# Kernel tuning notes

Hardware: AMD Instinct MI355X
Metric: run time of the kernel (lower is better)

The kernel has to match this reference:

```python
import jax, jax.numpy as jnp
import numpy as np

INPUT_DIM, DIM_K, DIM_V = 1024, 512, 512

def setup_inputs() -> dict:
    key = jax.random.key(0)
    kx, kq, kk, kv = jax.random.split(key, 4)
    x = jax.random.normal(kx, (4, 4096, INPUT_DIM), dtype=jnp.float32)
    s = 1.0 / np.sqrt(INPUT_DIM)
    Wq = jax.random.normal(kq, (INPUT_DIM, DIM_K), dtype=jnp.float32) * s
    Wk = jax.random.normal(kk, (INPUT_DIM, DIM_K), dtype=jnp.float32) * s
    Wv = jax.random.normal(kv, (INPUT_DIM, DIM_V), dtype=jnp.float32) * s
    return {"x": x, "Wq": Wq, "Wk": Wk, "Wv": Wv}

def reference(x, Wq, Wk, Wv):
    # x: [b, n, d_in]; bias-free projections
    Q = jnp.einsum('bnd,dk->bnk', x, Wq)
    K = jnp.einsum('bnd,dk->bnk', x, Wk)
    V = jnp.einsum('bnd,dv->bnv', x, Wv)
    scale = 1.0 / np.sqrt(Wq.shape[1])
    scores = jnp.einsum('bqk,bnk->bqn', Q, K) * scale  # [b, n, n]
    atten = jax.nn.softmax(scores, axis=-1)
    return jnp.einsum('bqn,bnv->bqv', atten, V)
```

## Files before the change

### kernel.cpp

```cpp
#include <hip/hip_runtime.h>
#include <hip/hip_bf16.h>


typedef __attribute__((ext_vector_type(8))) short bf16x8;
typedef __attribute__((ext_vector_type(4))) float floatx4;

static __device__ __forceinline__ unsigned short f2bf(float f) {
    unsigned int u = __builtin_bit_cast(unsigned int, f);
    return (unsigned short)((u + 0x7fffu + ((u >> 16) & 1u)) >> 16);
}

static __device__ __forceinline__ void gl2lds16(const unsigned short* g, unsigned short* l) {
    __builtin_amdgcn_global_load_lds(
        (const __attribute__((address_space(1))) unsigned int*)g,
        (__attribute__((address_space(3))) unsigned int*)l, 16, 0, 0);
}

#define BAR() __asm__ volatile("s_barrier" ::: "memory")
#define WVMC4() __asm__ volatile("s_waitcnt vmcnt(4)" ::: "memory")
#define WVMC0() __asm__ volatile("s_waitcnt vmcnt(0)" ::: "memory")
#define WLGKM0() __asm__ volatile("s_waitcnt lgkmcnt(0)" ::: "memory")
#define WALL() __asm__ volatile("s_waitcnt vmcnt(0) lgkmcnt(0)" ::: "memory")

__global__ __launch_bounds__(256) void cvt_bf16(const float* __restrict__ X,
                                                unsigned short* __restrict__ Y, int n4) {
    int i = blockIdx.x * 256 + threadIdx.x;
    if (i < n4) {
        float4 v = reinterpret_cast<const float4*>(X)[i];
        ushort4 o;
        o.x = f2bf(v.x); o.y = f2bf(v.y); o.z = f2bf(v.z); o.w = f2bf(v.w);
        reinterpret_cast<ushort4*>(Y)[i] = o;
    }
}

__global__ __launch_bounds__(256) void transpose_w(const float* __restrict__ W,
                                                   unsigned short* __restrict__ Wt, int off) {
    __shared__ float tile[32][33];
    int n0 = blockIdx.x * 32;
    int k0 = blockIdx.y * 32;
    int tx = threadIdx.x & 31, ty = threadIdx.x >> 5;
    for (int i = 0; i < 32; i += 8)
        tile[ty + i][tx] = W[(size_t)(k0 + ty + i) * 512 + n0 + tx];
    __syncthreads();
    for (int i = 0; i < 32; i += 8)
        Wt[(size_t)(off + n0 + ty + i) * 1024 + k0 + tx] = f2bf(tile[tx][ty + i]);
}

__global__ __launch_bounds__(256) void gemm_qkv(const unsigned short* __restrict__ A,
                                                const unsigned short* __restrict__ Bt,
                                                unsigned short* __restrict__ Qb,
                                                unsigned short* __restrict__ Kfr,
                                                unsigned short* __restrict__ Vfr) {
    __shared__ unsigned short As[128 * 32];
    __shared__ unsigned short Bs[128 * 32];
    const int K = 1024;
    const int L = blockIdx.x;
    const int mt = ((L & 7) << 4) | ((L >> 3) & 15);
    const int nt = L >> 7;
    const int m0 = mt * 128, n0 = nt * 128;
    const int tid = threadIdx.x;
    const int lane = tid & 63, wave = tid >> 6;
    const int wm = (wave >> 1) * 64, wn = (wave & 1) * 64;
    const int quad = lane >> 4, l15 = lane & 15;

    floatx4 acc[4][4] = {};
    const int srow = tid >> 2, scol = (tid & 3) * 8;

    for (int kt = 0; kt < K; kt += 32) {
        const unsigned short* ga = A + (size_t)(m0 + srow) * K + kt + scol;
        const unsigned short* gb = Bt + (size_t)(n0 + srow) * K + kt + scol;
        gl2lds16(ga, As + tid * 8);
        gl2lds16(ga + (size_t)64 * K, As + 2048 + tid * 8);
        gl2lds16(gb, Bs + tid * 8);
        gl2lds16(gb + (size_t)64 * K, Bs + 2048 + tid * 8);
        __syncthreads();
        bf16x8 af[4], bfr[4];
#pragma unroll
        for (int i = 0; i < 4; i++)
            af[i] = *reinterpret_cast<const bf16x8*>(As + (wm + i * 16 + l15) * 32 + quad * 8);
#pragma unroll
        for (int j = 0; j < 4; j++)
            bfr[j] = *reinterpret_cast<const bf16x8*>(Bs + (wn + j * 16 + l15) * 32 + quad * 8);
#pragma unroll
        for (int i = 0; i < 4; i++)
#pragma unroll
            for (int j = 0; j < 4; j++)
                acc[i][j] = __builtin_amdgcn_mfma_f32_16x16x32_bf16(af[i], bfr[j], acc[i][j], 0, 0, 0);
        __syncthreads();
    }

    const float qscale = 0.044194173824159216f;
#pragma unroll
    for (int i = 0; i < 4; i++)
#pragma unroll
        for (int j = 0; j < 4; j++)
#pragma unroll
            for (int r = 0; r < 4; r++) {
                int row = m0 + wm + i * 16 + quad * 4 + r;
                int col = n0 + wn + j * 16 + l15;
                if (n0 < 512) {
                    Qb[(size_t)row * 512 + col] = f2bf(acc[i][j][r] * qscale);
                } else if (n0 < 1024) {
                    int d = col - 512;
                    size_t base = ((size_t)((row >> 12) * 128 + ((row & 4095) >> 5))) << 14;
                    int off = ((d >> 5) * 2 + ((row >> 4) & 1)) * 512 +
                              (((d >> 3) & 3) * 16 + (row & 15)) * 8 + (d & 7);
                    Kfr[base + off] = f2bf(acc[i][j][r]);
                } else {
                    int d = col - 1024;
                    size_t base = ((size_t)((row >> 12) * 128 + ((row & 4095) >> 5))) << 14;
                    int off = (d >> 4) * 512 +
                              (((row & 31) >> 3) * 16 + (d & 15)) * 8 + (row & 7);
                    Vfr[base + off] = f2bf(acc[i][j][r]);
                }
            }
}

__global__ __launch_bounds__(512, 2) void attn(const unsigned short* __restrict__ Qg,
                                               const unsigned short* __restrict__ Kf,
                                               const unsigned short* __restrict__ Vf,
                                               float* __restrict__ O0,
                                               float* __restrict__ O1,
                                               float* __restrict__ lpart) {
    __shared__ unsigned short Kb[16384];
    __shared__ unsigned short Vb[3][16384];
    __shared__ unsigned short Ps[2][8][512];

    const int L = blockIdx.x;
    const int b = L & 3;
    const int h = (L >> 2) & 1;
    const int q0 = (L >> 3) * 128;
    const int tid = threadIdx.x;
    const int lane = tid & 63, wave = tid >> 6;
    const int quad = lane >> 4, l15 = lane & 15;
    const int qh = wave >> 2, dq = wave & 3;

    const unsigned short* KfB = Kf + ((size_t)b << 21);
    const unsigned short* VfB = Vf + ((size_t)b << 21);
    float* Od = (h == 0) ? O0 : O1;

    bf16x8 qf[16];
    {
        const unsigned short* qrow =
            Qg + (size_t)(b * 4096 + q0 + wave * 16 + l15) * 512 + quad * 8;
#pragma unroll
        for (int ks = 0; ks < 16; ks++)
            qf[ks] = *reinterpret_cast<const bf16x8*>(qrow + ks * 32);
    }
    WALL();

    floatx4 o[4][8];
#pragma unroll
    for (int g = 0; g < 4; g++)
#pragma unroll
        for (int n2 = 0; n2 < 8; n2++) o[g][n2] = floatx4{0.f, 0.f, 0.f, 0.f};
    float lp = 0.f;

    const int kt0 = h * 64;
    {
        const unsigned short* gK = KfB + ((size_t)kt0 << 14);
#pragma unroll
        for (int i = 0; i < 4; i++)
            gl2lds16(gK + (i * 512 + tid) * 8, &Kb[(i * 512 + tid) * 8]);
    }

    int vs = 0;
    for (int it = 0; it < 64; it++) {
        {
            const unsigned short* gV = VfB + ((size_t)(kt0 + it) << 14);
#pragma unroll
            for (int i = 0; i < 4; i++)
                gl2lds16(gV + (i * 512 + tid) * 8, &Vb[vs][(i * 512 + tid) * 8]);
        }
        WVMC4();
        BAR();

        const unsigned short* Kc = &Kb[0];
        floatx4 s00 = {0.f,0.f,0.f,0.f}, s01 = {0.f,0.f,0.f,0.f};
        floatx4 s10 = {0.f,0.f,0.f,0.f}, s11 = {0.f,0.f,0.f,0.f};
        __builtin_amdgcn_s_setprio(1);
#pragma unroll
        for (int ks = 0; ks < 16; ks += 2) {
            bf16x8 k0a = *reinterpret_cast<const bf16x8*>(Kc + (2 * ks + 0) * 512 + lane * 8);
            bf16x8 k1a = *reinterpret_cast<const bf16x8*>(Kc + (2 * ks + 1) * 512 + lane * 8);
            bf16x8 k0b = *reinterpret_cast<const bf16x8*>(Kc + (2 * ks + 2) * 512 + lane * 8);
            bf16x8 k1b = *reinterpret_cast<const bf16x8*>(Kc + (2 * ks + 3) * 512 + lane * 8);
            s00 = __builtin_amdgcn_mfma_f32_16x16x32_bf16(k0a, qf[ks], s00, 0, 0, 0);
            s10 = __builtin_amdgcn_mfma_f32_16x16x32_bf16(k1a, qf[ks], s10, 0, 0, 0);
            s01 = __builtin_amdgcn_mfma_f32_16x16x32_bf16(k0b, qf[ks + 1], s01, 0, 0, 0);
            s11 = __builtin_amdgcn_mfma_f32_16x16x32_bf16(k1b, qf[ks + 1], s11, 0, 0, 0);
        }
        __builtin_amdgcn_s_setprio(0);
        floatx4 s0v = s00 + s01, s1v = s10 + s11;

        {
            float p0[4], p1[4];
#pragma unroll
            for (int r = 0; r < 4; r++) {
                p0[r] = __expf(s0v[r] - 16.0f);
                p1[r] = __expf(s1v[r] - 16.0f);
                lp += p0[r] + p1[r];
            }
            unsigned int a0, a1, b0, b1;
            asm("v_cvt_pk_bf16_f32 %0, %1, %2" : "=v"(a0) : "v"(p0[0]), "v"(p0[1]));
            asm("v_cvt_pk_bf16_f32 %0, %1, %2" : "=v"(a1) : "v"(p0[2]), "v"(p0[3]));
            asm("v_cvt_pk_bf16_f32 %0, %1, %2" : "=v"(b0) : "v"(p1[0]), "v"(p1[1]));
            asm("v_cvt_pk_bf16_f32 %0, %1, %2" : "=v"(b1) : "v"(p1[2]), "v"(p1[3]));
            unsigned short* Pw = &Ps[it & 1][wave][0];
            const int wo = (quad >> 1) * 128 + l15 * 8 + (quad & 1) * 4;
            *reinterpret_cast<uint2*>(Pw + wo)       = uint2{a0, a1};
            *reinterpret_cast<uint2*>(Pw + wo + 256) = uint2{b0, b1};
        }
        WLGKM0();
        WVMC0();
        BAR();

        {
            const unsigned short* gK = KfB + ((size_t)(kt0 + ((it + 1) & 63)) << 14);
#pragma unroll
            for (int i = 0; i < 4; i++)
                gl2lds16(gK + (i * 512 + tid) * 8, &Kb[(i * 512 + tid) * 8]);
        }

        const unsigned short* Vc = &Vb[vs][0];
        bf16x8 vfr[8];
#pragma unroll
        for (int n2 = 0; n2 < 8; n2++)
            vfr[n2] = *reinterpret_cast<const bf16x8*>(Vc + (dq * 8 + n2) * 512 + lane * 8);
        __builtin_amdgcn_s_setprio(1);
#pragma unroll
        for (int g = 0; g < 4; g++) {
            bf16x8 pf = *reinterpret_cast<const bf16x8*>(&Ps[it & 1][qh * 4 + g][0] + lane * 8);
#pragma unroll
            for (int n2 = 0; n2 < 8; n2++)
                o[g][n2] = __builtin_amdgcn_mfma_f32_16x16x32_bf16(pf, vfr[n2], o[g][n2], 0, 0, 0);
        }
        __builtin_amdgcn_s_setprio(0);

        vs = (vs == 2) ? 0 : vs + 1;
    }
    WALL();

    lp += __shfl_xor(lp, 16);
    lp += __shfl_xor(lp, 32);
    if (quad == 0)
        lpart[h * 16384 + b * 4096 + q0 + wave * 16 + l15] = lp;

#pragma unroll
    for (int g = 0; g < 4; g++)
#pragma unroll
        for (int r = 0; r < 4; r++) {
            size_t rowoff = (size_t)(b * 4096 + q0 + qh * 64 + g * 16 + quad * 4 + r) * 512
                            + dq * 128 + l15;
#pragma unroll
            for (int n2 = 0; n2 < 8; n2++)
                Od[rowoff + n2 * 16] = o[g][n2][r];
        }
}

__global__ __launch_bounds__(256) void combine(float* __restrict__ Out,
                                               const float* __restrict__ O1,
                                               const float* __restrict__ lpart) {
    int i = blockIdx.x * 256 + threadIdx.x;
    int row = i >> 7;
    float inv = 1.0f / (lpart[row] + lpart[16384 + row]);
    float4 a = reinterpret_cast<const float4*>(Out)[i];
    float4 c = reinterpret_cast<const float4*>(O1)[i];
    float4 r;
    r.x = (a.x + c.x) * inv;
    r.y = (a.y + c.y) * inv;
    r.z = (a.z + c.z) * inv;
    r.w = (a.w + c.w) * inv;
    reinterpret_cast<float4*>(Out)[i] = r;
}

extern "C" void kernel_launch(void* const* d_in, const int* in_sizes, int n_in,
                              void* d_out, int out_size, void* d_ws, size_t ws_size,
                              hipStream_t stream) {
    const float* x  = (const float*)d_in[0];
    const float* Wq = (const float*)d_in[1];
    const float* Wk = (const float*)d_in[2];
    const float* Wv = (const float*)d_in[3];

    char* ws = (char*)d_ws;
    unsigned short* Wtall = (unsigned short*)(ws);
    unsigned short* Qb  = (unsigned short*)(ws + (3u << 20));
    unsigned short* Kfr = (unsigned short*)(ws + (19u << 20));
    unsigned short* Vfr = (unsigned short*)(ws + (35u << 20));
    unsigned short* xb  = (unsigned short*)(ws + (51u << 20));
    float* O1    = (float*)(ws + (51u << 20));
    float* lpart = (float*)(ws + (83u << 20));

    dim3 tb(256);
    cvt_bf16<<<dim3(16384), tb, 0, stream>>>(x, xb, 16384 * 1024 / 4);
    transpose_w<<<dim3(16, 32), tb, 0, stream>>>(Wq, Wtall, 0);
    transpose_w<<<dim3(16, 32), tb, 0, stream>>>(Wk, Wtall, 512);
    transpose_w<<<dim3(16, 32), tb, 0, stream>>>(Wv, Wtall, 1024);
    gemm_qkv<<<dim3(1536), tb, 0, stream>>>(xb, Wtall, Qb, Kfr, Vfr);
    attn<<<dim3(256), dim3(512), 0, stream>>>(Qb, Kfr, Vfr, (float*)d_out, O1, lpart);
    combine<<<dim3(8192), tb, 0, stream>>>((float*)d_out, O1, lpart);
}
```

Baseline: 341.3 us.

## Rewrite QKV GEMM with 256x192 tiles, swizzled LDS and multi-stage prefetch

The QKV projection GEMM moves from 128x128 tiles with a single-buffered K loop of 32 to 256x192 tiles with 512 threads and a K step of 64. A operands are triple-buffered and B operands double-buffered in an XOR-swizzled LDS layout, with staged global-to-LDS loads interleaved between MFMA phases and wave priority raised around the MFMA blocks. The three weight-transpose launches are merged into one 3D-grid launch. The aim is to hide global load latency, cut LDS bank conflicts and raise arithmetic intensity, at the cost of more LDS, more registers and more complex barrier sequencing.

```diff
diff --git a/kernel.cpp b/kernel.cpp
--- a/kernel.cpp
+++ b/kernel.cpp
@@ -33,9 +33,13 @@
     }
 }
 
-__global__ __launch_bounds__(256) void transpose_w(const float* __restrict__ W,
-                                                   unsigned short* __restrict__ Wt, int off) {
+__global__ __launch_bounds__(256) void transpose_w3(const float* __restrict__ Wq,
+                                                    const float* __restrict__ Wk,
+                                                    const float* __restrict__ Wv,
+                                                    unsigned short* __restrict__ Wt) {
     __shared__ float tile[32][33];
+    const float* W = (blockIdx.z == 0) ? Wq : (blockIdx.z == 1) ? Wk : Wv;
+    const int off = blockIdx.z << 9;
     int n0 = blockIdx.x * 32;
     int k0 = blockIdx.y * 32;
     int tx = threadIdx.x & 31, ty = threadIdx.x >> 5;
@@ -46,72 +50,153 @@
         Wt[(size_t)(off + n0 + ty + i) * 1024 + k0 + tx] = f2bf(tile[tx][ty + i]);
 }
 
-__global__ __launch_bounds__(256) void gemm_qkv(const unsigned short* __restrict__ A,
-                                                const unsigned short* __restrict__ Bt,
-                                                unsigned short* __restrict__ Qb,
-                                                unsigned short* __restrict__ Kfr,
-                                                unsigned short* __restrict__ Vfr) {
-    __shared__ unsigned short As[128 * 32];
-    __shared__ unsigned short Bs[128 * 32];
-    const int K = 1024;
+__global__ __launch_bounds__(512, 2) void gemm_qkv(const unsigned short* __restrict__ A,
+                                                   const unsigned short* __restrict__ Bt,
+                                                   unsigned short* __restrict__ Qb,
+                                                   unsigned short* __restrict__ Kfr,
+                                                   unsigned short* __restrict__ Vfr) {
+    __shared__ unsigned short AsU[3 * 16384];
+    __shared__ unsigned short BsU[2 * 12288];
+
     const int L = blockIdx.x;
-    const int mt = ((L & 7) << 4) | ((L >> 3) & 15);
-    const int nt = L >> 7;
-    const int m0 = mt * 128, n0 = nt * 128;
+    const int i6 = L >> 3;
+    const int mt = ((L & 7) << 3) | (i6 >> 3);
+    const int nt = i6 & 7;
+    const int m0 = mt << 8, n0 = nt * 192;
     const int tid = threadIdx.x;
     const int lane = tid & 63, wave = tid >> 6;
-    const int wm = (wave >> 1) * 64, wn = (wave & 1) * 64;
+    const int wmi = wave >> 2, wni = wave & 3;
     const int quad = lane >> 4, l15 = lane & 15;
 
-    floatx4 acc[4][4] = {};
-    const int srow = tid >> 2, scol = (tid & 3) * 8;
-
-    for (int kt = 0; kt < K; kt += 32) {
-        const unsigned short* ga = A + (size_t)(m0 + srow) * K + kt + scol;
-        const unsigned short* gb = Bt + (size_t)(n0 + srow) * K + kt + scol;
-        gl2lds16(ga, As + tid * 8);
-        gl2lds16(ga + (size_t)64 * K, As + 2048 + tid * 8);
-        gl2lds16(gb, Bs + tid * 8);
-        gl2lds16(gb + (size_t)64 * K, Bs + 2048 + tid * 8);
-        __syncthreads();
-        bf16x8 af[4], bfr[4];
-#pragma unroll
-        for (int i = 0; i < 4; i++)
-            af[i] = *reinterpret_cast<const bf16x8*>(As + (wm + i * 16 + l15) * 32 + quad * 8);
-#pragma unroll
-        for (int j = 0; j < 4; j++)
-            bfr[j] = *reinterpret_cast<const bf16x8*>(Bs + (wn + j * 16 + l15) * 32 + quad * 8);
-#pragma unroll
-        for (int i = 0; i < 4; i++)
-#pragma unroll
-            for (int j = 0; j < 4; j++)
-                acc[i][j] = __builtin_amdgcn_mfma_f32_16x16x32_bf16(af[i], bfr[j], acc[i][j], 0, 0, 0);
-        __syncthreads();
-    }
+    const int srow = tid >> 3;
+    const int sslot = (tid & 7) ^ ((tid >> 3) & 7);
+
+    auto stageA = [&](int slot, int ktile, int c) {
+        const unsigned short* src =
+            A + (size_t)(m0 + c * 64 + srow) * 1024 + (ktile << 6) + sslot * 8;
+        gl2lds16(src, AsU + slot * 16384 + c * 4096 + tid * 8);
+    };
+    auto stageB = [&](int slot, int ktile, int c) {
+        const unsigned short* src =
+            Bt + (size_t)(n0 + c * 64 + srow) * 1024 + (ktile << 6) + sslot * 8;
+        gl2lds16(src, BsU + slot * 12288 + c * 4096 + tid * 8);
+    };
+
+    floatx4 acc[8][3] = {};
+
+    for (int c = 0; c < 4; c++) stageA(0, 0, c);
+    for (int c = 0; c < 3; c++) stageB(0, 0, c);
+    for (int c = 0; c < 4; c++) stageA(1, 1, c);
+    WVMC4();
+    BAR();
+
+    int cura = 0, curb = 0;
+    for (int j = 0; j < 16; ++j) {
+        const int nb = curb ^ 1;
+        const int na = (cura >= 1) ? cura - 1 : cura + 2;
+        const int ktB = (j + 1) & 15, ktA = (j + 2) & 15;
+        const unsigned short* Ab = AsU + cura * 16384;
+        const unsigned short* Bb = BsU + curb * 12288;
+
+        bf16x8 af[4], bfr[3];
+        const int arow = (wmi << 7) + l15;
+        const int brow = wni * 48 + l15;
+        const int sw = l15 & 7;
+
+#pragma unroll
+        for (int f = 0; f < 4; f++)
+            af[f] = *reinterpret_cast<const bf16x8*>(Ab + (arow + f * 16) * 64 + (quad ^ sw) * 8);
+#pragma unroll
+        for (int f = 0; f < 3; f++)
+            bfr[f] = *reinterpret_cast<const bf16x8*>(Bb + (brow + f * 16) * 64 + (quad ^ sw) * 8);
+        stageB(nb, ktB, 0);
+        stageB(nb, ktB, 1);
+        BAR();
+        __builtin_amdgcn_s_setprio(1);
+#pragma unroll
+        for (int f = 0; f < 4; f++)
+#pragma unroll
+            for (int g = 0; g < 3; g++)
+                acc[f][g] = __builtin_amdgcn_mfma_f32_16x16x32_bf16(af[f], bfr[g], acc[f][g], 0, 0, 0);
+        __builtin_amdgcn_s_setprio(0);
+        BAR();
+
+#pragma unroll
+        for (int f = 0; f < 4; f++)
+            af[f] = *reinterpret_cast<const bf16x8*>(Ab + (arow + (f + 4) * 16) * 64 + (quad ^ sw) * 8);
+        stageB(nb, ktB, 2);
+        stageA(na, ktA, 0);
+        BAR();
+        __builtin_amdgcn_s_setprio(1);
+#pragma unroll
+        for (int f = 0; f < 4; f++)
+#pragma unroll
+            for (int g = 0; g < 3; g++)
+                acc[f + 4][g] = __builtin_amdgcn_mfma_f32_16x16x32_bf16(af[f], bfr[g], acc[f + 4][g], 0, 0, 0);
+        __builtin_amdgcn_s_setprio(0);
+        BAR();
+
+#pragma unroll
+        for (int f = 0; f < 4; f++)
+            af[f] = *reinterpret_cast<const bf16x8*>(Ab + (arow + f * 16) * 64 + ((4 + quad) ^ sw) * 8);
+#pragma unroll
+        for (int f = 0; f < 3; f++)
+            bfr[f] = *reinterpret_cast<const bf16x8*>(Bb + (brow + f * 16) * 64 + ((4 + quad) ^ sw) * 8);
+        stageA(na, ktA, 1);
+        stageA(na, ktA, 2);
+        BAR();
+        __builtin_amdgcn_s_setprio(1);
+#pragma unroll
+        for (int f = 0; f < 4; f++)
+#pragma unroll
+            for (int g = 0; g < 3; g++)
+                acc[f][g] = __builtin_amdgcn_mfma_f32_16x16x32_bf16(af[f], bfr[g], acc[f][g], 0, 0, 0);
+        __builtin_amdgcn_s_setprio(0);
+        BAR();
+
+#pragma unroll
+        for (int f = 0; f < 4; f++)
+            af[f] = *reinterpret_cast<const bf16x8*>(Ab + (arow + (f + 4) * 16) * 64 + ((4 + quad) ^ sw) * 8);
+        stageA(na, ktA, 3);
+        BAR();
+        __builtin_amdgcn_s_setprio(1);
+#pragma unroll
+        for (int f = 0; f < 4; f++)
+#pragma unroll
+            for (int g = 0; g < 3; g++)
+                acc[f + 4][g] = __builtin_amdgcn_mfma_f32_16x16x32_bf16(af[f], bfr[g], acc[f + 4][g], 0, 0, 0);
+        __builtin_amdgcn_s_setprio(0);
+        WVMC4();
+        BAR();
+
+        curb = nb;
+        cura = (cura == 2) ? 0 : cura + 1;
+    }
+    WALL();
 
     const float qscale = 0.044194173824159216f;
 #pragma unroll
-    for (int i = 0; i < 4; i++)
-#pragma unroll
-        for (int j = 0; j < 4; j++)
+    for (int fi = 0; fi < 8; fi++)
+#pragma unroll
+        for (int fj = 0; fj < 3; fj++)
 #pragma unroll
             for (int r = 0; r < 4; r++) {
-                int row = m0 + wm + i * 16 + quad * 4 + r;
-                int col = n0 + wn + j * 16 + l15;
-                if (n0 < 512) {
-                    Qb[(size_t)row * 512 + col] = f2bf(acc[i][j][r] * qscale);
-                } else if (n0 < 1024) {
+                int row = m0 + (wmi << 7) + fi * 16 + quad * 4 + r;
+                int col = n0 + wni * 48 + fj * 16 + l15;
+                if (col < 512) {
+                    Qb[(size_t)row * 512 + col] = f2bf(acc[fi][fj][r] * qscale);
+                } else if (col < 1024) {
                     int d = col - 512;
                     size_t base = ((size_t)((row >> 12) * 128 + ((row & 4095) >> 5))) << 14;
                     int off = ((d >> 5) * 2 + ((row >> 4) & 1)) * 512 +
                               (((d >> 3) & 3) * 16 + (row & 15)) * 8 + (d & 7);
-                    Kfr[base + off] = f2bf(acc[i][j][r]);
+                    Kfr[base + off] = f2bf(acc[fi][fj][r]);
                 } else {
                     int d = col - 1024;
                     size_t base = ((size_t)((row >> 12) * 128 + ((row & 4095) >> 5))) << 14;
                     int off = (d >> 4) * 512 +
                               (((row & 31) >> 3) * 16 + (d & 15)) * 8 + (row & 7);
-                    Vfr[base + off] = f2bf(acc[i][j][r]);
+                    Vfr[base + off] = f2bf(acc[fi][fj][r]);
                 }
             }
 }
@@ -293,10 +378,8 @@
 
     dim3 tb(256);
     cvt_bf16<<<dim3(16384), tb, 0, stream>>>(x, xb, 16384 * 1024 / 4);
-    transpose_w<<<dim3(16, 32), tb, 0, stream>>>(Wq, Wtall, 0);
-    transpose_w<<<dim3(16, 32), tb, 0, stream>>>(Wk, Wtall, 512);
-    transpose_w<<<dim3(16, 32), tb, 0, stream>>>(Wv, Wtall, 1024);
-    gemm_qkv<<<dim3(1536), tb, 0, stream>>>(xb, Wtall, Qb, Kfr, Vfr);
+    transpose_w3<<<dim3(16, 32, 3), tb, 0, stream>>>(Wq, Wk, Wv, Wtall);
+    gemm_qkv<<<dim3(512), dim3(512), 0, stream>>>(xb, Wtall, Qb, Kfr, Vfr);
     attn<<<dim3(256), dim3(512), 0, stream>>>(Qb, Kfr, Vfr, (float*)d_out, O1, lpart);
     combine<<<dim3(8192), tb, 0, stream>>>((float*)d_out, O1, lpart);
 }
```

New measurement: 339.4 us. About the same (-0.5%).
